# Kernel tuning notes

Measured on AMD Instinct MI355X. Metric: run time of the kernel, lower is better.

Reference implementation:

```python
import jax, jax.numpy as jnp
import numpy as np

C_IN = 3; IMG = 256; LAT = 256; K = 1024; L = 4
ENC = [128, 256, 512]; DEC = [512, 256, 128]


def conv2d(x, w, b, stride, pad):
    # x: NCHW, w: OIHW
    y = jax.lax.conv_general_dilated(x, w, (stride, stride), [(pad, pad), (pad, pad)],
                                     dimension_numbers=('NCHW', 'OIHW', 'NCHW'))
    return y + b[None, :, None, None]


def convT(x, w, b):
    # stride-2 transposed conv, kernel 4, 'SAME' -> doubles H,W. w: HWIO
    y = jax.lax.conv_transpose(x, w, (2, 2), 'SAME',
                               dimension_numbers=('NCHW', 'HWIO', 'NCHW'))
    return y + b[None, :, None, None]


def setup_inputs() -> dict:
    key = jax.random.key(0)
    ks = iter(jax.random.split(key, 32))
    def w(shape, fan_in):
        return jax.random.normal(next(ks), shape, jnp.float32) / np.float32(np.sqrt(fan_in))
    inp = {'x': jax.random.normal(next(ks), (8, C_IN, IMG, IMG), jnp.float32)}
    cin = C_IN
    for i, co in enumerate(ENC):
        inp[f'enc_w{i}'] = w((co, cin, 4, 4), cin * 16)
        inp[f'enc_b{i}'] = jnp.zeros((co,), jnp.float32)
        cin = co
    inp['proj_w'] = w((LAT, ENC[-1], 1, 1), ENC[-1])
    inp['proj_b'] = jnp.zeros((LAT,), jnp.float32)
    cin = LAT
    for i, co in enumerate(DEC):
        inp[f'dec_w{i}'] = w((4, 4, cin, co), cin * 16)
        inp[f'dec_b{i}'] = jnp.zeros((co,), jnp.float32)
        cin = co
    inp['out_w'] = w((C_IN, DEC[-1], 3, 3), DEC[-1] * 9)
    inp['out_b'] = jnp.zeros((C_IN,), jnp.float32)
    # per-level codebooks, uniform(-1/K, 1/K) as in the torch init
    inp['emb'] = jax.random.uniform(next(ks), (L, K, LAT), jnp.float32, -1.0 / K, 1.0 / K)
    return inp


def reference(x, enc_w0, enc_b0, enc_w1, enc_b1, enc_w2, enc_b2,
              proj_w, proj_b, dec_w0, dec_b0, dec_w1, dec_b1, dec_w2, dec_b2,
              out_w, out_b, emb):
    # encoder: three stride-2 convs + ReLU
    h = x
    for w_, b_ in ((enc_w0, enc_b0), (enc_w1, enc_b1), (enc_w2, enc_b2)):
        h = jax.nn.relu(conv2d(h, w_, b_, 2, 1))
    z = conv2d(h, proj_w, proj_b, 1, 0)  # [B, LAT, 32, 32]

    # residual quantization over L levels
    B, C, H, W = z.shape
    r = z
    z_q = jnp.zeros_like(z)
    residuals, codes = [], []
    for l in range(L):
        E = emb[l]                                   # [K, C]
        rf = r.transpose(0, 2, 3, 1).reshape(-1, C)  # [B*H*W, C]
        # squared euclidean distance (argmin equal to cdist argmin)
        d2 = (jnp.sum(rf * rf, axis=1, keepdims=True)
              - 2.0 * (rf @ E.T)
              + jnp.sum(E * E, axis=1))
        idx = jnp.argmin(d2, axis=1)                 # [B*H*W]
        e = E[idx].reshape(B, H, W, C).transpose(0, 3, 1, 2)
        residuals.append(r)
        codes.append(idx.reshape(B, H, W))
        z_q = z_q + e
        r = r - e

    # straight-through estimator
    z_q_st = z + jax.lax.stop_gradient(z_q - z)

    # decoder: three stride-2 transposed convs + ReLU, then 3x3 output conv
    d = z_q_st
    for w_, b_ in ((dec_w0, dec_b0), (dec_w1, dec_b1), (dec_w2, dec_b2)):
        d = jax.nn.relu(convT(d, w_, b_))
    recon = conv2d(d, out_w, out_b, 1, 1)  # [B, 3, 256, 256] == img_size, no interp
    return recon, z, z_q, jnp.stack(residuals), jnp.stack(codes)
```

## Files before the change

kernel.cpp:

```cpp
#include <hip/hip_runtime.h>
#include <hip/hip_bf16.h>
#include <cstdint>

#define BATCH 8
#define LATC 256
#define NCODE 1024
#define NLVL 4

typedef __attribute__((ext_vector_type(8))) short bf16x8v;
typedef __attribute__((ext_vector_type(4))) float f32x4v;

__device__ __forceinline__ unsigned short f2b(float f) {
  __hip_bfloat16 h = __float2bfloat16(f);
  return *reinterpret_cast<unsigned short*>(&h);
}

__device__ __forceinline__ void gl_lds16(const void* gptr, unsigned lds_byte_off) {
  unsigned m0v = __builtin_amdgcn_readfirstlane(lds_byte_off);
  asm volatile("s_mov_b32 m0, %0\n"
               "global_load_lds_dwordx4 %1, off\n" ::"s"(m0v), "v"(gptr)
               : "memory");
}

template <int CIN, int COUT, int HIN, int CI_CHUNK, int CO_TILE, int CI_SPLIT>
__global__ __launch_bounds__(256) void conv_enc(
    const float* __restrict__ in, const float* __restrict__ w,
    const float* __restrict__ bias, float* __restrict__ out) {
  constexpr int WIN = HIN;
  constexpr int HOUT = HIN / 2, WOUT = WIN / 2;
  constexpr int PT1 = HOUT / 16;
  constexpr int CPW = CO_TILE / 4;
  constexpr int CL = CPW / 4;
  constexpr int NEL = CI_CHUNK * 34 * 34;
  constexpr int WUNITS = CI_CHUNK * CO_TILE * 4;
  constexpr int CIPS = CIN / CI_SPLIT;

  __shared__ float T[CI_CHUNK][34][36];
  __shared__ float4 Wsh[CI_CHUNK][CO_TILE][4];

  const int tid = threadIdx.x;
  const int lane = tid & 63;
  const int wv = __builtin_amdgcn_readfirstlane(tid >> 6);
  const int opy = (lane >> 3) << 1;
  const int bq = lane & 7;
  const int opx = bq << 1;

  const int bx = blockIdx.x;
  const int n = bx / (PT1 * PT1);
  const int pt = bx % (PT1 * PT1);
  const int oh0 = (pt / PT1) * 16, ow0 = (pt % PT1) * 16;
  const int hbase = 2 * oh0 - 1, wbase = 2 * ow0 - 1;
  const int co_blk = blockIdx.y * CO_TILE;
  const int co_base = co_blk + wv * CPW;
  const int split = (CI_SPLIT > 1) ? blockIdx.z : 0;
  const int ci_base = split * CIPS;

  float acc[CL][4][2][2];
#pragma unroll
  for (int cl = 0; cl < CL; ++cl)
#pragma unroll
    for (int j = 0; j < 4; ++j) {
      float b = (CI_SPLIT == 1 || split == 0) ? bias[co_base + cl * 4 + j] : 0.f;
      acc[cl][j][0][0] = b; acc[cl][j][0][1] = b;
      acc[cl][j][1][0] = b; acc[cl][j][1][1] = b;
    }

  for (int ch = ci_base; ch < ci_base + CIPS; ch += CI_CHUNK) {
    for (int u = tid; u < NEL; u += 256) {
      int cir = u / 1156;
      int rem = u - cir * 1156;
      int r = rem / 34, c = rem - r * 34;
      int hi = hbase + r, wi = wbase + c;
      float v = 0.f;
      if ((unsigned)hi < (unsigned)HIN && (unsigned)wi < (unsigned)WIN)
        v = in[((long long)(n * CIN + ch + cir) * HIN + hi) * WIN + wi];
      T[cir][r][c] = v;
    }
    for (int u = tid; u < WUNITS; u += 256) {
      int k4 = u & 3;
      int rem = u >> 2;
      int co = rem % CO_TILE, ci = rem / CO_TILE;
      Wsh[ci][co][k4] =
          *(const float4*)&w[((long long)(co_blk + co) * CIN + ch + ci) * 16 + k4 * 4];
    }
    __syncthreads();
#pragma unroll
    for (int cir = 0; cir < CI_CHUNK; ++cir) {
      float xv[6][6];
#pragma unroll
      for (int r = 0; r < 6; ++r) {
        float4 qa = *(const float4*)&T[cir][2 * opy + r][4 * bq];
        float4 qb = *(const float4*)&T[cir][2 * opy + r][4 * bq + 4];
        xv[r][0] = qa.x; xv[r][1] = qa.y; xv[r][2] = qa.z; xv[r][3] = qa.w;
        xv[r][4] = qb.x; xv[r][5] = qb.y;
      }
#pragma unroll
      for (int cl = 0; cl < CL; ++cl)
#pragma unroll
        for (int j = 0; j < 4; ++j) {
          int co_l = wv * CPW + cl * 4 + j;
#pragma unroll
          for (int kh = 0; kh < 4; ++kh) {
            float4 wq = Wsh[cir][co_l][kh];
            float wt0 = wq.x, wt1 = wq.y, wt2 = wq.z, wt3 = wq.w;
#pragma unroll
            for (int dy = 0; dy < 2; ++dy)
#pragma unroll
              for (int dx = 0; dx < 2; ++dx) {
                acc[cl][j][dy][dx] = fmaf(xv[2 * dy + kh][2 * dx + 0], wt0, acc[cl][j][dy][dx]);
                acc[cl][j][dy][dx] = fmaf(xv[2 * dy + kh][2 * dx + 1], wt1, acc[cl][j][dy][dx]);
                acc[cl][j][dy][dx] = fmaf(xv[2 * dy + kh][2 * dx + 2], wt2, acc[cl][j][dy][dx]);
                acc[cl][j][dy][dx] = fmaf(xv[2 * dy + kh][2 * dx + 3], wt3, acc[cl][j][dy][dx]);
              }
          }
        }
    }
    __syncthreads();
  }
  const long long psz = (long long)BATCH * COUT * HOUT * WOUT;
  float* __restrict__ ob_ptr = out + (CI_SPLIT > 1 ? (long long)split * psz : 0LL);
#pragma unroll
  for (int cl = 0; cl < CL; ++cl)
#pragma unroll
    for (int j = 0; j < 4; ++j) {
      int co = co_base + cl * 4 + j;
#pragma unroll
      for (int dy = 0; dy < 2; ++dy) {
        int oh = oh0 + opy + dy, ow = ow0 + opx;
        float v0 = acc[cl][j][dy][0];
        float v1 = acc[cl][j][dy][1];
        if (CI_SPLIT == 1) { v0 = fmaxf(v0, 0.f); v1 = fmaxf(v1, 0.f); }
        *reinterpret_cast<float2*>(
            &ob_ptr[((long long)(n * COUT + co) * HOUT + oh) * WOUT + ow]) =
            make_float2(v0, v1);
      }
    }
}

template <int S, bool RELU>
__global__ __launch_bounds__(256) void fuse_sum(const float* __restrict__ p,
                                                float* __restrict__ out, long long n4) {
  long long i = (long long)blockIdx.x * 256 + threadIdx.x;
  long long stride = (long long)gridDim.x * 256;
  long long N = n4 * 4;
  for (; i < n4; i += stride) {
    float4 a = *(const float4*)&p[i * 4];
#pragma unroll
    for (int s = 1; s < S; ++s) {
      float4 b = *(const float4*)&p[(long long)s * N + i * 4];
      a.x += b.x; a.y += b.y; a.z += b.z; a.w += b.w;
    }
    if (RELU) {
      a.x = fmaxf(a.x, 0.f); a.y = fmaxf(a.y, 0.f);
      a.z = fmaxf(a.z, 0.f); a.w = fmaxf(a.w, 0.f);
    }
    *(float4*)&out[i * 4] = a;
  }
}

__global__ __launch_bounds__(256) void wtrans(const float* __restrict__ pw,
                                              float* __restrict__ pwT) {
  int gid = blockIdx.x * 256 + threadIdx.x;
  if (gid >= 512 * 256) return;
  int ci = gid >> 8, co = gid & 255;
  pwT[gid] = pw[co * 512 + ci];
}

template <int CI_SPLIT>
__global__ __launch_bounds__(256) void conv1x1_v2(
    const float* __restrict__ in, const float* __restrict__ pwT,
    const float* __restrict__ bias, float* __restrict__ out) {
  constexpr int CIPS = 512 / CI_SPLIT;
  __shared__ float Tx[16][128];
  const int tid = threadIdx.x;
  const int lane = tid & 63;
  const int wv = __builtin_amdgcn_readfirstlane(tid >> 6);
  const int p0 = lane * 2;
  const int bx = blockIdx.x;
  const int n = bx >> 3, pxb = bx & 7;
  const int px_base = pxb * 128;
  const int co_base = blockIdx.y * 64 + wv * 16;
  const int split = (CI_SPLIT > 1) ? blockIdx.z : 0;
  const int ci0 = split * CIPS;

  float acc[4][4][2];
#pragma unroll
  for (int cl = 0; cl < 4; ++cl)
#pragma unroll
    for (int j = 0; j < 4; ++j) {
      float b = (CI_SPLIT == 1 || split == 0) ? bias[co_base + cl * 4 + j] : 0.f;
      acc[cl][j][0] = b; acc[cl][j][1] = b;
    }

  for (int ch = ci0; ch < ci0 + CIPS; ch += 16) {
    for (int u = tid; u < 2048; u += 256) {
      int cir = u >> 7, p = u & 127;
      Tx[cir][p] = in[(long long)(n * 512 + ch + cir) * 1024 + px_base + p];
    }
    __syncthreads();
#pragma unroll
    for (int cir = 0; cir < 16; ++cir) {
      float2 xv = *reinterpret_cast<const float2*>(&Tx[cir][p0]);
#pragma unroll
      for (int cl = 0; cl < 4; ++cl) {
        const float* __restrict__ wp = pwT + (ch + cir) * 256 + co_base + cl * 4;
#pragma unroll
        for (int j = 0; j < 4; ++j) {
          float wt = wp[j];
          acc[cl][j][0] = fmaf(xv.x, wt, acc[cl][j][0]);
          acc[cl][j][1] = fmaf(xv.y, wt, acc[cl][j][1]);
        }
      }
    }
    __syncthreads();
  }
  const long long psz = (long long)BATCH * 256 * 1024;
  float* __restrict__ ob = out + (CI_SPLIT > 1 ? (long long)split * psz : 0LL);
#pragma unroll
  for (int cl = 0; cl < 4; ++cl)
#pragma unroll
    for (int j = 0; j < 4; ++j) {
      int co = co_base + cl * 4 + j;
      *reinterpret_cast<float2*>(&ob[(long long)(n * 256 + co) * 1024 + px_base + p0]) =
          make_float2(acc[cl][j][0], acc[cl][j][1]);
    }
}

__global__ __launch_bounds__(256) void emb_norms(
    const float* __restrict__ emb, float* __restrict__ en) {
  int k = blockIdx.x * blockDim.x + threadIdx.x;
  if (k >= NLVL * NCODE) return;
  const float* __restrict__ e = emb + (long long)k * LATC;
  float s = 0.f;
  for (int c = 0; c < LATC; ++c) s = fmaf(e[c], e[c], s);
  en[k] = s;
}

#define RQ_P 32
#define RQ_CT 32
#define RQ_RS 260

__global__ __launch_bounds__(256) void rq_kernel2(
    const float* __restrict__ z, const float* __restrict__ emb,
    const float* __restrict__ en, float* __restrict__ zq_out,
    float* __restrict__ resid_out, float* __restrict__ codes_out) {
  __shared__ float e_sh[RQ_CT * RQ_RS];
  __shared__ float r_sh[RQ_P * RQ_RS];
  __shared__ float sum_sh[RQ_P];
  __shared__ int code_sh[RQ_P];
  const int tid = threadIdx.x;
  const int blk = blockIdx.x;
  const int n = (blk * RQ_P) >> 10;
  const int hw0 = (blk * RQ_P) & 1023;
  const long long zb = ((long long)n * LATC) * 1024 + hw0;

  for (int it = 0; it < 32; ++it) {
    int u = it * 256 + tid;
    int c = u >> 5, pix = u & 31;
    float v = z[zb + (long long)c * 1024 + pix];
    r_sh[pix * RQ_RS + c] = v;
    resid_out[((long long)n * LATC + c) * 1024 + hw0 + pix] = v;
  }
  __syncthreads();

  const int code_l = tid & 31;
  const int pixoff = tid >> 5;
  const int upix = tid >> 3;
  const int ucg = tid & 7;

  for (int l = 0; l < NLVL; ++l) {
    {
      float s = 0.f;
#pragma unroll
      for (int it = 0; it < 8; ++it) {
        int c4 = ucg + it * 8;
        float4 r4 = *(const float4*)&r_sh[upix * RQ_RS + c4 * 4];
        s += r4.x * r4.x + r4.y * r4.y + r4.z * r4.z + r4.w * r4.w;
      }
      s += __shfl_xor(s, 1); s += __shfl_xor(s, 2); s += __shfl_xor(s, 4);
      if (ucg == 0) sum_sh[upix] = s;
    }
    __syncthreads();
    const float* __restrict__ E = emb + (long long)l * NCODE * LATC;
    const float* __restrict__ enl = en + l * NCODE;
    float best[4]; int bidx[4];
#pragma unroll
    for (int g = 0; g < 4; ++g) { best[g] = 3.4e38f; bidx[g] = 0; }
    for (int tile = 0; tile < NCODE / RQ_CT; ++tile) {
      const float* __restrict__ Et = E + (long long)tile * RQ_CT * LATC;
      for (int it = 0; it < 32; ++it) {
        int u = it * 256 + tid;
        int cc = u >> 8, ch = u & 255;
        e_sh[cc * RQ_RS + ch] = Et[cc * LATC + ch];
      }
      __syncthreads();
      float acc[4] = {0.f, 0.f, 0.f, 0.f};
      for (int c4 = 0; c4 < 64; ++c4) {
        float4 e4 = *(const float4*)&e_sh[code_l * RQ_RS + c4 * 4];
#pragma unroll
        for (int g = 0; g < 4; ++g) {
          float4 r4 = *(const float4*)&r_sh[(g * 8 + pixoff) * RQ_RS + c4 * 4];
          acc[g] = fmaf(r4.x, e4.x, acc[g]);
          acc[g] = fmaf(r4.y, e4.y, acc[g]);
          acc[g] = fmaf(r4.z, e4.z, acc[g]);
          acc[g] = fmaf(r4.w, e4.w, acc[g]);
        }
      }
      int code = tile * RQ_CT + code_l;
      float ek2 = enl[code];
#pragma unroll
      for (int g = 0; g < 4; ++g) {
        float d2 = (sum_sh[g * 8 + pixoff] - 2.f * acc[g]) + ek2;
        if (d2 < best[g]) { best[g] = d2; bidx[g] = code; }
      }
      __syncthreads();
    }
#pragma unroll
    for (int g = 0; g < 4; ++g) {
      float bd = best[g]; int bi = bidx[g];
#pragma unroll
      for (int m = 1; m < 32; m <<= 1) {
        float od = __shfl_xor(bd, m);
        int oi = __shfl_xor(bi, m);
        if (od < bd || (od == bd && oi < bi)) { bd = od; bi = oi; }
      }
      if (code_l == 0) {
        int pix = g * 8 + pixoff;
        code_sh[pix] = bi;
        codes_out[(long long)(l * BATCH + n) * 1024 + hw0 + pix] = (float)bi;
      }
    }
    __syncthreads();
    {
      int sel = code_sh[upix];
      const float* __restrict__ esel = E + (long long)sel * LATC;
#pragma unroll
      for (int it = 0; it < 8; ++it) {
        int c4 = ucg + it * 8;
        float4 r4 = *(const float4*)&r_sh[upix * RQ_RS + c4 * 4];
        float4 e4 = *(const float4*)&esel[c4 * 4];
        r4.x -= e4.x; r4.y -= e4.y; r4.z -= e4.z; r4.w -= e4.w;
        *(float4*)&r_sh[upix * RQ_RS + c4 * 4] = r4;
        if (l < NLVL - 1) {
          long long rb = ((long long)((l + 1) * BATCH + n) * LATC + c4 * 4) * 1024 + hw0 + upix;
          resid_out[rb] = r4.x;
          resid_out[rb + 1024] = r4.y;
          resid_out[rb + 2048] = r4.z;
          resid_out[rb + 3072] = r4.w;
        }
      }
    }
    __syncthreads();
  }
  for (int it = 0; it < 32; ++it) {
    int u = it * 256 + tid;
    int c = u >> 5, pix = u & 31;
    float zv = z[zb + (long long)c * 1024 + pix];
    zq_out[zb + (long long)c * 1024 + pix] = zv - r_sh[pix * RQ_RS + c];
  }
}

__global__ __launch_bounds__(256) void to_nhwc_s1(const float* __restrict__ zq,
                                                  unsigned short* __restrict__ o) {
  __shared__ float tsh[32][33];
  int bx = blockIdx.x;
  int ct = bx & 7, y = (bx >> 3) & 31, n = bx >> 8;
  int tid = threadIdx.x;
  int x = tid & 31, cl = tid >> 5;
#pragma unroll
  for (int it = 0; it < 4; ++it) {
    int ci = it * 8 + cl;
    tsh[ci][x] = zq[((long long)(n * 256 + ct * 32 + ci) * 32 + y) * 32 + x];
  }
  __syncthreads();
  int ci = tid & 31, xg = tid >> 5;
#pragma unroll
  for (int it = 0; it < 4; ++it) {
    int xw = it * 8 + xg;
    o[(((long long)n * 34 + y + 1) * 34 + xw + 1) * 256 + ct * 32 + ci] = f2b(tsh[ci][xw]);
  }
}

__global__ __launch_bounds__(256) void wprep_k(const float* __restrict__ w,
                                               unsigned short* __restrict__ o,
                                               int CINc, int COUTc) {
  long long total = 16LL * CINc * COUTc;
  long long gid = (long long)blockIdx.x * 256 + threadIdx.x;
  if (gid >= total) return;
  int ci32 = (int)(gid & 31); long long t = gid >> 5;
  int co = (int)(t % COUTc); t /= COUTc;
  int tap = (int)(t & 3); t >>= 2;
  int nch = CINc / 32;
  int ch = (int)(t % nch); int phase = (int)(t / nch);
  int py = phase >> 1, px = phase & 1;
  int ky = py + 2 * (tap >> 1), kx = px + 2 * (tap & 1);
  int ci = ch * 32 + ci32;
  float v = w[(((long long)ky * 4 + kx) * CINc + ci) * COUTc + co];
  o[gid] = f2b(v);
}

template <int CIN, int COUT, int TH, int TW, int Hi, int Wi, bool OUT_NCHW>
__global__ __launch_bounds__(256) void convt2(
    const unsigned short* __restrict__ xin, const unsigned short* __restrict__ wprep,
    const float* __restrict__ bias, unsigned short* __restrict__ outp) {
  constexpr int TWP = TW + 2, ROWS = TH + 2;
  constexpr int Hp = Hi + 2, Wp = Wi + 2;
  constexpr int NCH = CIN / 32;
  constexpr int XUNITS = ROWS * TWP;
  constexpr int XPAD = ((XUNITS + 255) / 256) * 256;
  constexpr int WBASE = 4 * XPAD;
  __shared__ unsigned short lds[(4 * XPAD + 4 * 256) * 8];

  const int tid = threadIdx.x;
  const int wv = tid >> 6, lane = tid & 63;
  const int l15 = lane & 15, seg = lane >> 4;

  constexpr int SW = Wi / TW, SH = Hi / TH;
  const int bx = blockIdx.x;
  const int n = bx / (SH * SW);
  const int srem = bx % (SH * SW);
  const int i0 = (srem / SW) * TH, j0 = (srem % SW) * TW;
  const int cob0 = blockIdx.y * 64;
  const int phase = blockIdx.z;
  const int pyp = phase >> 1, pxp = phase & 1;

  const unsigned short* xsrc = xin + (long long)n * Hp * Wp * CIN;

  f32x4v acc[4][4];
  if (!OUT_NCHW) {
#pragma unroll
    for (int b = 0; b < 4; ++b) {
      float bv = bias[cob0 + b * 16 + l15];
      f32x4v v = {bv, bv, bv, bv};
#pragma unroll
      for (int a = 0; a < 4; ++a) acc[a][b] = v;
    }
  } else {
#pragma unroll
    for (int a = 0; a < 4; ++a) {
      f32x4v v;
#pragma unroll
      for (int q = 0; q < 4; ++q) v[q] = bias[cob0 + a * 16 + seg * 4 + q];
#pragma unroll
      for (int b = 0; b < 4; ++b) acc[a][b] = v;
    }
  }

  for (int ch = 0; ch < NCH; ++ch) {
    __syncthreads();
#pragma unroll
    for (int sg = 0; sg < 4; ++sg) {
#pragma unroll
      for (int it = 0; it < XPAD / 256; ++it) {
        int u = it * 256 + tid;
        int us = u < XUNITS ? u : XUNITS - 1;
        int row = us / TWP, col = us % TWP;
        const unsigned short* g =
            xsrc + ((long long)(i0 + row) * Wp + (j0 + col)) * CIN + ch * 32 + sg * 8;
        gl_lds16(g, (unsigned)(unsigned long long)(const void*)&lds[(sg * XPAD + u) * 8]);
      }
    }
    {
      const unsigned short* wb = wprep + ((long long)phase * NCH + ch) * 4 * COUT * 32;
      int tap = tid >> 6, co = tid & 63;
#pragma unroll
      for (int sg = 0; sg < 4; ++sg) {
        const unsigned short* g = wb + ((long long)tap * COUT + cob0 + co) * 32 + sg * 8;
        gl_lds16(g, (unsigned)(unsigned long long)(const void*)&lds[(WBASE + sg * 256 + tid) * 8]);
      }
    }
    asm volatile("s_waitcnt vmcnt(0)" ::: "memory");
    __syncthreads();
#pragma unroll
    for (int t = 0; t < 4; ++t) {
      int oy = (t >> 1) - 1 + pyp, ox = (t & 1) - 1 + pxp;
      bf16x8v xf[4], wf[4];
#pragma unroll
      for (int i = 0; i < 4; ++i) {
        int p = wv * 64 + i * 16 + l15;
        int r = p / TW, c = p % TW;
        int xrow = r + oy + 1, xcol = c + ox + 1;
        xf[i] = *(const bf16x8v*)&lds[(seg * XPAD + xrow * TWP + xcol) * 8];
        wf[i] = *(const bf16x8v*)&lds[(WBASE + seg * 256 + t * 64 + i * 16 + l15) * 8];
      }
#pragma unroll
      for (int a = 0; a < 4; ++a)
#pragma unroll
        for (int b = 0; b < 4; ++b) {
          if (OUT_NCHW)
            acc[a][b] = __builtin_amdgcn_mfma_f32_16x16x32_bf16(wf[a], xf[b], acc[a][b], 0, 0, 0);
          else
            acc[a][b] = __builtin_amdgcn_mfma_f32_16x16x32_bf16(xf[a], wf[b], acc[a][b], 0, 0, 0);
        }
    }
  }

  if (!OUT_NCHW) {
    constexpr int Wpo = 2 * Wi + 2;
    long long ob_n = (long long)n * (2 * Hi + 2) * Wpo * COUT;
#pragma unroll
    for (int a = 0; a < 4; ++a)
#pragma unroll
      for (int q = 0; q < 4; ++q) {
        int p = wv * 64 + a * 16 + seg * 4 + q;
        int r = p / TW, c = p % TW;
        int yo = 2 * (i0 + r) + pyp + 1, xo = 2 * (j0 + c) + pxp + 1;
        long long ob = ob_n + ((long long)yo * Wpo + xo) * COUT + cob0;
#pragma unroll
        for (int b = 0; b < 4; ++b) {
          float v = fmaxf(acc[a][b][q], 0.f);
          outp[ob + b * 16 + l15] = f2b(v);
        }
      }
  } else {
    constexpr int Ho = 2 * Hi, Wo = 2 * Wi;
#pragma unroll
    for (int a = 0; a < 4; ++a)
#pragma unroll
      for (int q = 0; q < 4; ++q) {
        int co = cob0 + a * 16 + seg * 4 + q;
#pragma unroll
        for (int b = 0; b < 4; ++b) {
          int p = wv * 64 + b * 16 + l15;
          int r = p / TW, c = p % TW;
          int yo = 2 * (i0 + r) + pyp, xo = 2 * (j0 + c) + pxp;
          float v = fmaxf(acc[a][b][q], 0.f);
          outp[((long long)(n * COUT + co) * Ho + yo) * Wo + xo] = f2b(v);
        }
      }
  }
}

__global__ __launch_bounds__(256) void conv3x3_v2(
    const __hip_bfloat16* __restrict__ in, const float* __restrict__ w,
    const float* __restrict__ bias, float* __restrict__ out) {
  constexpr int H = 256, W = 256, CIN = 128;
  __shared__ float Wsh[3 * CIN * 9];
  __shared__ float T[4][34][35];

  const int tid = threadIdx.x;
  for (int u = tid; u < 3 * CIN * 9; u += 256) Wsh[u] = w[u];

  const int bx = blockIdx.x;
  const int n = bx >> 6;
  const int t8 = bx & 63;
  const int y0 = (t8 >> 3) * 32, x0 = (t8 & 7) * 32;
  const int ty = (tid >> 4) * 2;
  const int tx = (tid & 15) * 2;

  float acc[3][2][2];
#pragma unroll
  for (int co = 0; co < 3; ++co) {
    float b = bias[co];
    acc[co][0][0] = b; acc[co][0][1] = b; acc[co][1][0] = b; acc[co][1][1] = b;
  }

  for (int ch = 0; ch < CIN; ch += 4) {
    __syncthreads();
    for (int u = tid; u < 4 * 34 * 34; u += 256) {
      int ci = u / (34 * 34);
      int rem = u % (34 * 34);
      int r = rem / 34, c = rem % 34;
      int yy = y0 + r - 1, xx = x0 + c - 1;
      float v = 0.f;
      if ((unsigned)yy < (unsigned)H && (unsigned)xx < (unsigned)W)
        v = __bfloat162float(in[((long long)(n * CIN + ch + ci) * H + yy) * W + xx]);
      T[ci][r][c] = v;
    }
    __syncthreads();
#pragma unroll
    for (int ci = 0; ci < 4; ++ci) {
      float xv[4][4];
#pragma unroll
      for (int r = 0; r < 4; ++r)
#pragma unroll
        for (int c = 0; c < 4; ++c) xv[r][c] = T[ci][ty + r][tx + c];
#pragma unroll
      for (int co = 0; co < 3; ++co) {
        const float* __restrict__ wp = &Wsh[(co * CIN + ch + ci) * 9];
#pragma unroll
        for (int kh = 0; kh < 3; ++kh)
#pragma unroll
          for (int kw = 0; kw < 3; ++kw) {
            float wt = wp[kh * 3 + kw];
            acc[co][0][0] = fmaf(xv[kh][kw], wt, acc[co][0][0]);
            acc[co][0][1] = fmaf(xv[kh][kw + 1], wt, acc[co][0][1]);
            acc[co][1][0] = fmaf(xv[kh + 1][kw], wt, acc[co][1][0]);
            acc[co][1][1] = fmaf(xv[kh + 1][kw + 1], wt, acc[co][1][1]);
          }
      }
    }
  }
#pragma unroll
  for (int co = 0; co < 3; ++co)
#pragma unroll
    for (int dy = 0; dy < 2; ++dy) {
      long long ob = ((long long)(n * 3 + co) * H + y0 + ty + dy) * W + x0 + tx;
      *reinterpret_cast<float2*>(&out[ob]) = make_float2(acc[co][dy][0], acc[co][dy][1]);
    }
}

extern "C" void kernel_launch(void* const* d_in, const int* in_sizes, int n_in,
                              void* d_out, int out_size, void* d_ws, size_t ws_size,
                              hipStream_t stream) {
  const float* x   = (const float*)d_in[0];
  const float* ew0 = (const float*)d_in[1];  const float* eb0 = (const float*)d_in[2];
  const float* ew1 = (const float*)d_in[3];  const float* eb1 = (const float*)d_in[4];
  const float* ew2 = (const float*)d_in[5];  const float* eb2 = (const float*)d_in[6];
  const float* pw  = (const float*)d_in[7];  const float* pb  = (const float*)d_in[8];
  const float* dw0 = (const float*)d_in[9];  const float* db0 = (const float*)d_in[10];
  const float* dw1 = (const float*)d_in[11]; const float* db1 = (const float*)d_in[12];
  const float* dw2 = (const float*)d_in[13]; const float* db2 = (const float*)d_in[14];
  const float* ow  = (const float*)d_in[15]; const float* ob  = (const float*)d_in[16];
  const float* emb = (const float*)d_in[17];

  float* out   = (float*)d_out;
  float* recon = out;
  float* z     = out + 1572864;
  float* zq    = out + 3670016;
  float* resid = out + 5767168;
  float* codes = out + 14155776;

  char* ws = (char*)d_ws;
  dim3 blk(256);
  auto g = [](long long tot) { return dim3((unsigned)((tot + 255) / 256)); };

  const size_t OFF_S1IN  = 0ULL;
  const size_t OFF_S1OUT = 4734976ULL;
  const size_t OFF_WP1   = 40419328ULL;
  const size_t OFF_WP2   = 44613632ULL;
  const size_t OFF_P     = 67108864ULL;
  const size_t OFF_E2    = 134217728ULL;
  const size_t OFF_PWT   = 150994944ULL;
  const size_t OFF_DD2   = 0ULL;
  const size_t OFF_S2OUT = 134217728ULL;
  const size_t OFF_WP3   = 203440128ULL;
  const size_t OFF_EN    = 204488704ULL;
  const size_t WS_NEED   = 204505088ULL;

  if (ws_size < WS_NEED) return;

  float* e0  = (float*)(ws);
  float* p2  = (float*)(ws + OFF_P);
  float* e1  = (float*)(ws);
  float* p3  = (float*)(ws + OFF_P);
  float* e2  = (float*)(ws + OFF_E2);
  float* q1  = (float*)(ws + OFF_P);
  float* en  = (float*)(ws + OFF_EN);
  float* pwT = (float*)(ws + OFF_PWT);
  unsigned short* s1in  = (unsigned short*)(ws + OFF_S1IN);
  unsigned short* s1out = (unsigned short*)(ws + OFF_S1OUT);
  unsigned short* s2out = (unsigned short*)(ws + OFF_S2OUT);
  unsigned short* dd2   = (unsigned short*)(ws + OFF_DD2);
  unsigned short* wp1   = (unsigned short*)(ws + OFF_WP1);
  unsigned short* wp2   = (unsigned short*)(ws + OFF_WP2);
  unsigned short* wp3   = (unsigned short*)(ws + OFF_WP3);

  emb_norms<<<g(4096), blk, 0, stream>>>(emb, en);

  conv_enc<3, 128, 256, 3, 64, 1><<<dim3(512, 2, 1), blk, 0, stream>>>(x, ew0, eb0, e0);
  conv_enc<128, 256, 128, 4, 64, 4><<<dim3(128, 4, 4), blk, 0, stream>>>(e0, ew1, eb1, p2);
  fuse_sum<4, true><<<dim3(4096), blk, 0, stream>>>(p2, e1, 8388608 / 4);
  conv_enc<256, 512, 64, 4, 32, 4><<<dim3(32, 16, 4), blk, 0, stream>>>(e1, ew2, eb2, p3);
  fuse_sum<4, true><<<dim3(2048), blk, 0, stream>>>(p3, e2, 4194304 / 4);
  wtrans<<<g(512 * 256), blk, 0, stream>>>(pw, pwT);
  conv1x1_v2<4><<<dim3(64, 4, 4), blk, 0, stream>>>(e2, pwT, pb, q1);
  fuse_sum<4, false><<<dim3(1024), blk, 0, stream>>>(q1, z, 2097152 / 4);

  rq_kernel2<<<dim3(256), blk, 0, stream>>>(z, emb, en, zq, resid, codes);

  hipMemsetAsync(ws + OFF_S1IN, 0, 4734976ULL, stream);
  hipMemsetAsync(ws + OFF_S1OUT, 0, 35684352ULL, stream);
  hipMemsetAsync(ws + OFF_S2OUT, 0, 69222400ULL, stream);
  to_nhwc_s1<<<dim3(2048), blk, 0, stream>>>(zq, s1in);
  wprep_k<<<g(16LL * 256 * 512), blk, 0, stream>>>(dw0, wp1, 256, 512);
  wprep_k<<<g(16LL * 512 * 256), blk, 0, stream>>>(dw1, wp2, 512, 256);
  wprep_k<<<g(16LL * 256 * 128), blk, 0, stream>>>(dw2, wp3, 256, 128);

  convt2<256, 512, 8, 32, 32, 32, false>
      <<<dim3(32, 8, 4), dim3(256), 0, stream>>>(s1in, wp1, db0, s1out);
  convt2<512, 256, 4, 64, 64, 64, false>
      <<<dim3(128, 4, 4), dim3(256), 0, stream>>>(s1out, wp2, db1, s2out);
  convt2<256, 128, 4, 64, 128, 128, true>
      <<<dim3(512, 2, 4), dim3(256), 0, stream>>>(s2out, wp3, db2, dd2);

  conv3x3_v2<<<dim3(512), blk, 0, stream>>>((const __hip_bfloat16*)dd2, ow, ob, recon);
}
```

Measured before the change: 2.917 ms.

## Remap encoder conv threads to 8 channels by 2x4 pixels with padded LDS rows

Rewrites the encoder stride-2 conv so each lane computes a 2x4 pixel patch for 8 output channels, instead of 2x2 pixels across all of the wave's channels. Input rows in LDS get an extra 4-float offset on alternating row groups to avoid bank conflicts on the wider 10-float reads. Stores become float4. The third encoder layer now uses a 64-channel tile with half the grid in y. The aim is more FMAs per LDS load and fewer weight reads per lane, in exchange for more LDS and register use per thread.

```diff
diff --git a/kernel.cpp b/kernel.cpp
--- a/kernel.cpp
+++ b/kernel.cpp
@@ -23,27 +23,27 @@
 }
 
 template <int CIN, int COUT, int HIN, int CI_CHUNK, int CO_TILE, int CI_SPLIT>
-__global__ __launch_bounds__(256) void conv_enc(
+__global__ __launch_bounds__(256) void conv_enc2(
     const float* __restrict__ in, const float* __restrict__ w,
     const float* __restrict__ bias, float* __restrict__ out) {
   constexpr int WIN = HIN;
   constexpr int HOUT = HIN / 2, WOUT = WIN / 2;
   constexpr int PT1 = HOUT / 16;
-  constexpr int CPW = CO_TILE / 4;
-  constexpr int CL = CPW / 4;
   constexpr int NEL = CI_CHUNK * 34 * 34;
   constexpr int WUNITS = CI_CHUNK * CO_TILE * 4;
   constexpr int CIPS = CIN / CI_SPLIT;
 
-  __shared__ float T[CI_CHUNK][34][36];
+  __shared__ float T[CI_CHUNK][34][40];
   __shared__ float4 Wsh[CI_CHUNK][CO_TILE][4];
 
   const int tid = threadIdx.x;
   const int lane = tid & 63;
   const int wv = __builtin_amdgcn_readfirstlane(tid >> 6);
-  const int opy = (lane >> 3) << 1;
-  const int bq = lane & 7;
-  const int opx = bq << 1;
+  const int cog = lane >> 5;
+  const int pxi = lane & 31;
+  const int m = pxi >> 2;
+  const int ox4 = pxi & 3;
+  const int co_loc0 = (wv * 2 + cog) * 8;
 
   const int bx = blockIdx.x;
   const int n = bx / (PT1 * PT1);
@@ -51,18 +51,19 @@
   const int oh0 = (pt / PT1) * 16, ow0 = (pt % PT1) * 16;
   const int hbase = 2 * oh0 - 1, wbase = 2 * ow0 - 1;
   const int co_blk = blockIdx.y * CO_TILE;
-  const int co_base = co_blk + wv * CPW;
   const int split = (CI_SPLIT > 1) ? blockIdx.z : 0;
   const int ci_base = split * CIPS;
 
-  float acc[CL][4][2][2];
-#pragma unroll
-  for (int cl = 0; cl < CL; ++cl)
+  float acc[2][4][2][4];
+#pragma unroll
+  for (int cl = 0; cl < 2; ++cl)
 #pragma unroll
     for (int j = 0; j < 4; ++j) {
-      float b = (CI_SPLIT == 1 || split == 0) ? bias[co_base + cl * 4 + j] : 0.f;
-      acc[cl][j][0][0] = b; acc[cl][j][0][1] = b;
-      acc[cl][j][1][0] = b; acc[cl][j][1][1] = b;
+      float b = (CI_SPLIT == 1 || split == 0) ? bias[co_blk + co_loc0 + cl * 4 + j] : 0.f;
+#pragma unroll
+      for (int dy = 0; dy < 2; ++dy)
+#pragma unroll
+        for (int dx = 0; dx < 4; ++dx) acc[cl][j][dy][dx] = b;
     }
 
   for (int ch = ci_base; ch < ci_base + CIPS; ch += CI_CHUNK) {
@@ -74,7 +75,7 @@
       float v = 0.f;
       if ((unsigned)hi < (unsigned)HIN && (unsigned)wi < (unsigned)WIN)
         v = in[((long long)(n * CIN + ch + cir) * HIN + hi) * WIN + wi];
-      T[cir][r][c] = v;
+      T[cir][r][(((r >> 2) & 1) << 2) + c] = v;
     }
     for (int u = tid; u < WUNITS; u += 256) {
       int k4 = u & 3;
@@ -86,32 +87,38 @@
     __syncthreads();
 #pragma unroll
     for (int cir = 0; cir < CI_CHUNK; ++cir) {
-      float xv[6][6];
-#pragma unroll
-      for (int r = 0; r < 6; ++r) {
-        float4 qa = *(const float4*)&T[cir][2 * opy + r][4 * bq];
-        float4 qb = *(const float4*)&T[cir][2 * opy + r][4 * bq + 4];
-        xv[r][0] = qa.x; xv[r][1] = qa.y; xv[r][2] = qa.z; xv[r][3] = qa.w;
-        xv[r][4] = qb.x; xv[r][5] = qb.y;
-      }
-#pragma unroll
-      for (int cl = 0; cl < CL; ++cl)
+      float xv[6][10];
+#pragma unroll
+      for (int roff = 0; roff < 6; ++roff) {
+        int row = 4 * m + roff;
+        const float* base = &T[cir][row][(((row >> 2) & 1) << 2) + 8 * ox4];
+        float4 qa = *(const float4*)base;
+        float4 qb = *(const float4*)(base + 4);
+        float4 qc = *(const float4*)(base + 8);
+        xv[roff][0] = qa.x; xv[roff][1] = qa.y; xv[roff][2] = qa.z; xv[roff][3] = qa.w;
+        xv[roff][4] = qb.x; xv[roff][5] = qb.y; xv[roff][6] = qb.z; xv[roff][7] = qb.w;
+        xv[roff][8] = qc.x; xv[roff][9] = qc.y;
+      }
+#pragma unroll
+      for (int cl = 0; cl < 2; ++cl)
 #pragma unroll
         for (int j = 0; j < 4; ++j) {
-          int co_l = wv * CPW + cl * 4 + j;
+          int co_l = co_loc0 + cl * 4 + j;
 #pragma unroll
           for (int kh = 0; kh < 4; ++kh) {
             float4 wq = Wsh[cir][co_l][kh];
             float wt0 = wq.x, wt1 = wq.y, wt2 = wq.z, wt3 = wq.w;
 #pragma unroll
-            for (int dy = 0; dy < 2; ++dy)
-#pragma unroll
-              for (int dx = 0; dx < 2; ++dx) {
-                acc[cl][j][dy][dx] = fmaf(xv[2 * dy + kh][2 * dx + 0], wt0, acc[cl][j][dy][dx]);
-                acc[cl][j][dy][dx] = fmaf(xv[2 * dy + kh][2 * dx + 1], wt1, acc[cl][j][dy][dx]);
-                acc[cl][j][dy][dx] = fmaf(xv[2 * dy + kh][2 * dx + 2], wt2, acc[cl][j][dy][dx]);
-                acc[cl][j][dy][dx] = fmaf(xv[2 * dy + kh][2 * dx + 3], wt3, acc[cl][j][dy][dx]);
+            for (int dy = 0; dy < 2; ++dy) {
+              int r = 2 * dy + kh;
+#pragma unroll
+              for (int dx = 0; dx < 4; ++dx) {
+                acc[cl][j][dy][dx] = fmaf(xv[r][2 * dx + 0], wt0, acc[cl][j][dy][dx]);
+                acc[cl][j][dy][dx] = fmaf(xv[r][2 * dx + 1], wt1, acc[cl][j][dy][dx]);
+                acc[cl][j][dy][dx] = fmaf(xv[r][2 * dx + 2], wt2, acc[cl][j][dy][dx]);
+                acc[cl][j][dy][dx] = fmaf(xv[r][2 * dx + 3], wt3, acc[cl][j][dy][dx]);
               }
+            }
           }
         }
     }
@@ -120,19 +127,22 @@
   const long long psz = (long long)BATCH * COUT * HOUT * WOUT;
   float* __restrict__ ob_ptr = out + (CI_SPLIT > 1 ? (long long)split * psz : 0LL);
 #pragma unroll
-  for (int cl = 0; cl < CL; ++cl)
+  for (int cl = 0; cl < 2; ++cl)
 #pragma unroll
     for (int j = 0; j < 4; ++j) {
-      int co = co_base + cl * 4 + j;
+      int co = co_blk + co_loc0 + cl * 4 + j;
 #pragma unroll
       for (int dy = 0; dy < 2; ++dy) {
-        int oh = oh0 + opy + dy, ow = ow0 + opx;
-        float v0 = acc[cl][j][dy][0];
-        float v1 = acc[cl][j][dy][1];
-        if (CI_SPLIT == 1) { v0 = fmaxf(v0, 0.f); v1 = fmaxf(v1, 0.f); }
-        *reinterpret_cast<float2*>(
-            &ob_ptr[((long long)(n * COUT + co) * HOUT + oh) * WOUT + ow]) =
-            make_float2(v0, v1);
+        int oh = oh0 + 2 * m + dy, ow = ow0 + 4 * ox4;
+        float4 v;
+#pragma unroll
+        for (int dx = 0; dx < 4; ++dx) {
+          float t = acc[cl][j][dy][dx];
+          if (CI_SPLIT == 1) t = fmaxf(t, 0.f);
+          ((float*)&v)[dx] = t;
+        }
+        *reinterpret_cast<float4*>(
+            &ob_ptr[((long long)(n * COUT + co) * HOUT + oh) * WOUT + ow]) = v;
       }
     }
 }
@@ -658,10 +668,10 @@
 
   emb_norms<<<g(4096), blk, 0, stream>>>(emb, en);
 
-  conv_enc<3, 128, 256, 3, 64, 1><<<dim3(512, 2, 1), blk, 0, stream>>>(x, ew0, eb0, e0);
-  conv_enc<128, 256, 128, 4, 64, 4><<<dim3(128, 4, 4), blk, 0, stream>>>(e0, ew1, eb1, p2);
+  conv_enc2<3, 128, 256, 3, 64, 1><<<dim3(512, 2, 1), blk, 0, stream>>>(x, ew0, eb0, e0);
+  conv_enc2<128, 256, 128, 4, 64, 4><<<dim3(128, 4, 4), blk, 0, stream>>>(e0, ew1, eb1, p2);
   fuse_sum<4, true><<<dim3(4096), blk, 0, stream>>>(p2, e1, 8388608 / 4);
-  conv_enc<256, 512, 64, 4, 32, 4><<<dim3(32, 16, 4), blk, 0, stream>>>(e1, ew2, eb2, p3);
+  conv_enc2<256, 512, 64, 4, 64, 4><<<dim3(32, 8, 4), blk, 0, stream>>>(e1, ew2, eb2, p3);
   fuse_sum<4, true><<<dim3(2048), blk, 0, stream>>>(p3, e2, 4194304 / 4);
   wtrans<<<g(512 * 256), blk, 0, stream>>>(pw, pwT);
   conv1x1_v2<4><<<dim3(64, 4, 4), blk, 0, stream>>>(e2, pwT, pb, q1);
```

New measurement: 2.777 ms. 4.8% less time.
